# Kernel tuning notes

Measured on AMD Instinct MI355X. Metric: run time of the kernel, lower is better.

Reference implementation:

```python
import jax, jax.numpy as jnp
import numpy as np

CH_W = (1.0, 0.5, 2.0)  # channel_weights from init
NUM_NODES, FEAT_DIM, EMBED_DIM, B = 1_000_000, 128, 128, 200_000


def setup_inputs() -> dict:
    key = jax.random.key(0)
    ks = jax.random.split(key, 10)
    return {
        "nodes": jax.random.randint(ks[0], (B,), 0, NUM_NODES, dtype=jnp.int64 if jax.config.jax_enable_x64 else jnp.int32),
        "features": jax.random.normal(ks[1], (NUM_NODES, FEAT_DIM), dtype=jnp.float32),
        "neigh0": jax.random.normal(ks[2], (B, FEAT_DIM), dtype=jnp.float32),
        "neigh1": jax.random.normal(ks[3], (B, FEAT_DIM), dtype=jnp.float32),
        "neigh2": jax.random.normal(ks[4], (B, FEAT_DIM), dtype=jnp.float32),
        "W1": jax.random.normal(ks[5], (FEAT_DIM, 4 * FEAT_DIM), dtype=jnp.float32) * 0.05,
        "b1": jax.random.normal(ks[6], (FEAT_DIM,), dtype=jnp.float32) * 0.05,
        "W2": jax.random.normal(ks[7], (EMBED_DIM, FEAT_DIM), dtype=jnp.float32) * 0.05,
        "b2": jax.random.normal(ks[8], (EMBED_DIM,), dtype=jnp.float32) * 0.05,
    }


def reference(nodes, features, neigh0, neigh1, neigh2, W1, b1, W2, b2):
    # gather self embeddings: features(LongTensor(nodes))
    self_feats = features[nodes]                                   # [B, F]
    # per-channel weight scaling then concat: [B, (C+1)*F]
    combined = jnp.concatenate(
        [self_feats, neigh0 * CH_W[0], neigh1 * CH_W[1], neigh2 * CH_W[2]], axis=1
    )
    # Linear -> Tanh -> Linear (torch Linear: x @ W.T + b)
    h = jnp.tanh(combined @ W1.T + b1)                             # [B, F]
    return h @ W2.T + b2                                           # [B, E]
```

## Files before the change

kernel.cpp:

```cpp
#include <hip/hip_runtime.h>
#include <hip/hip_bf16.h>

typedef __attribute__((ext_vector_type(8))) short bf16x8;
typedef __attribute__((ext_vector_type(4))) float f32x4;

__device__ __forceinline__ unsigned short f2bf(float x){
  union { float f; unsigned int u; } a; a.f = x;
  unsigned int r = a.u + 0x7FFFu + ((a.u >> 16) & 1u);
  return (unsigned short)(r >> 16);
}

__device__ __forceinline__ void glds16(const void* g, void* l){
  __builtin_amdgcn_global_load_lds(
      (const __attribute__((address_space(1))) unsigned int*)g,
      (__attribute__((address_space(3))) unsigned int*)l,
      16, 0, 0);
}

__global__ void prep_w(const float* __restrict__ W1, const float* __restrict__ W2,
                       unsigned short* __restrict__ W1p, unsigned short* __restrict__ W2p){
  int t = blockIdx.x * 256 + threadIdx.x;
  int lane = t & 63;
  int lo = lane & 15, hi = lane >> 4;
  {
    int ktg = (t >> 6) & 15, nt = t >> 10;
    int c = ktg >> 2;
    int base = (c==0) ? 2 : ((c==1) ? 0 : 2*c);
    int P = base + ((ktg >> 1) & 1);
    int k2 = ktg & 1;
    float s = (c==2) ? 0.5f : ((c==3) ? 2.0f : 1.0f);
    int n = nt*16 + lo;
    int k = ktg*32 + hi*8;
    const float* src = W1 + n*512 + k;
    unsigned short* dst = W1p + ((size_t)((P*8 + nt)*2 + k2)*64 + lane)*8;
#pragma unroll
    for (int j=0;j<8;j++) dst[j] = f2bf(src[j]*s);
  }
  if (t < 2048){
    int kt = (t >> 6) & 3, nt = t >> 8;
    int n = nt*16 + lo;
    int k = kt*32 + hi*8;
    const float* src = W2 + n*128 + k;
    unsigned short* dst = W2p + (size_t)t*8;
#pragma unroll
    for (int j=0;j<8;j++) dst[j] = f2bf(src[j]);
  }
}

__device__ __forceinline__ void stage_neigh(char* db, int wv, int lane, int brow,
                                            const float* g, int half, int B){
  int r4 = lane >> 4, gs = lane & 15;
#pragma unroll
  for (int j=0;j<4;j++){
    int row = 4*(wv*4 + j) + r4;
    int gr = brow + row; gr = gr < B ? gr : (B-1);
    const char* src = (const char*)(g + (size_t)gr*128 + half*64) + ((gs ^ (row & 7)) << 4);
    glds16(src, db + row*256 + (gs << 4));
  }
}
__device__ __forceinline__ void stage_gather(char* db, int wv, int lane,
                                             const float* feat, const int* nid, int half){
  int r4 = lane >> 4, gs = lane & 15;
#pragma unroll
  for (int j=0;j<4;j++){
    int row = 4*(wv*4 + j) + r4;
    const char* src = (const char*)(feat + (size_t)nid[j]*128 + half*64) + ((gs ^ (row & 7)) << 4);
    glds16(src, db + row*256 + (gs << 4));
  }
}
__device__ __forceinline__ void stage_w(char* wb, int wv, int lane,
                                        const unsigned short* W1p, int P){
  const char* src = (const char*)W1p + (size_t)P*16384 + (wv*4)*1024 + (lane << 4);
#pragma unroll
  for (int j=0;j<4;j++)
    glds16(src + j*1024, wb + (wv*4 + j)*1024 + (lane << 4));
}

__device__ __forceinline__ void gemm_phase(const char* db, const char* wb,
    int wv, int lo, int hi, int lane, f32x4 acc[8])
{
  int row = wv*16 + lo;
  int s = row & 7;
  const char* rb = db + row*256;
  bf16x8 a[2];
#pragma unroll
  for (int k2=0;k2<2;k2++){
    int g0 = (8*k2 + 2*hi) ^ s;
    float4 x = *(const float4*)(rb + (g0 << 4));
    float4 y = *(const float4*)(rb + ((g0 ^ 1) << 4));
    bf16x8 t;
    t[0]=(short)f2bf(x.x); t[1]=(short)f2bf(x.y); t[2]=(short)f2bf(x.z); t[3]=(short)f2bf(x.w);
    t[4]=(short)f2bf(y.x); t[5]=(short)f2bf(y.y); t[6]=(short)f2bf(y.z); t[7]=(short)f2bf(y.w);
    a[k2] = t;
  }
#pragma unroll
  for (int nt=0;nt<8;nt++){
#pragma unroll
    for (int k2=0;k2<2;k2++){
      bf16x8 b = *(const bf16x8*)(wb + (((nt*2 + k2)*64 + lane) << 4));
      acc[nt] = __builtin_amdgcn_mfma_f32_16x16x32_bf16(a[k2], b, acc[nt], 0, 0, 0);
    }
  }
}

#define PH_WAIT8 asm volatile("s_waitcnt vmcnt(8)" ::: "memory")
#define PH_WAIT0 asm volatile("s_waitcnt vmcnt(0)" ::: "memory")
#define BAR do{ asm volatile("" ::: "memory"); __builtin_amdgcn_s_barrier(); \
                asm volatile("" ::: "memory"); }while(0)

__global__ __launch_bounds__(256, 2) void enc_main(
    const int* __restrict__ nodes, const float* __restrict__ feat,
    const float* __restrict__ g0, const float* __restrict__ g1,
    const float* __restrict__ g2,
    const unsigned short* __restrict__ W1p, const float* __restrict__ b1,
    const unsigned short* __restrict__ W2p, const float* __restrict__ b2,
    float* __restrict__ out, int B)
{
  __shared__ char smem[65536];
  char* DB0 = smem;            char* DB1 = smem + 16384;
  char* WB0 = smem + 32768;    char* WB1 = smem + 49152;

  const int tid  = threadIdx.x;
  const int lane = tid & 63;
  const int wv   = tid >> 6;
  const int lo   = lane & 15, hi = lane >> 4;
  const int brow = blockIdx.x * 64;

  float bb1[8];
#pragma unroll
  for (int nt=0;nt<8;nt++) bb1[nt] = b1[lo + 16*nt];
  int nid[4];
  {
    int r4 = lane >> 4;
#pragma unroll
    for (int j=0;j<4;j++){
      int r = brow + 4*(wv*4 + j) + r4;
      r = r < B ? r : (B-1);
      nid[j] = nodes[r];
    }
  }
  asm volatile("" ::: "memory");

  stage_neigh(DB0, wv, lane, brow, g0, 0, B);  stage_w(WB0, wv, lane, W1p, 0);
  stage_neigh(DB1, wv, lane, brow, g0, 1, B);  stage_w(WB1, wv, lane, W1p, 1);

  f32x4 acc[8];
#pragma unroll
  for (int nt=0;nt<8;nt++) acc[nt] = (f32x4){bb1[nt],bb1[nt],bb1[nt],bb1[nt]};

  PH_WAIT8; BAR;
  gemm_phase(DB0, WB0, wv, lo, hi, lane, acc);
  BAR;
  stage_gather(DB0, wv, lane, feat, nid, 0);   stage_w(WB0, wv, lane, W1p, 2);
  PH_WAIT8; BAR;
  gemm_phase(DB1, WB1, wv, lo, hi, lane, acc);
  BAR;
  stage_gather(DB1, wv, lane, feat, nid, 1);   stage_w(WB1, wv, lane, W1p, 3);
  PH_WAIT8; BAR;
  gemm_phase(DB0, WB0, wv, lo, hi, lane, acc);
  BAR;
  stage_neigh(DB0, wv, lane, brow, g1, 0, B);  stage_w(WB0, wv, lane, W1p, 4);
  PH_WAIT8; BAR;
  gemm_phase(DB1, WB1, wv, lo, hi, lane, acc);
  BAR;
  stage_neigh(DB1, wv, lane, brow, g1, 1, B);  stage_w(WB1, wv, lane, W1p, 5);
  PH_WAIT8; BAR;
  gemm_phase(DB0, WB0, wv, lo, hi, lane, acc);
  BAR;
  stage_neigh(DB0, wv, lane, brow, g2, 0, B);  stage_w(WB0, wv, lane, W1p, 6);
  PH_WAIT8; BAR;
  gemm_phase(DB1, WB1, wv, lo, hi, lane, acc);
  BAR;
  stage_neigh(DB1, wv, lane, brow, g2, 1, B);  stage_w(WB1, wv, lane, W1p, 7);
  PH_WAIT8; BAR;
  gemm_phase(DB0, WB0, wv, lo, hi, lane, acc);
  BAR;
  PH_WAIT0; BAR;
  gemm_phase(DB1, WB1, wv, lo, hi, lane, acc);

  char* hbase = WB0 + wv*4096;
#pragma unroll
  for (int nt=0;nt<8;nt++){
#pragma unroll
    for (int r=0;r<4;r++){
      float x = acc[nt][r];
      float t = 1.0f - 2.0f * __builtin_amdgcn_rcpf(__expf(2.0f*x) + 1.0f);
      int row = hi*4 + r;
      int colb = (lo + 16*nt)*2;
      *(unsigned short*)(hbase + row*256 + (colb ^ ((row & 7) << 4))) = f2bf(t);
    }
  }
  __syncthreads();

  const bf16x8* W2f = (const bf16x8*)W2p;
  f32x4 acc2[8];
#pragma unroll
  for (int nt=0;nt<8;nt++){ float v2 = b2[lo + 16*nt]; acc2[nt] = (f32x4){v2,v2,v2,v2}; }

  bf16x8 a2[4];
  {
    int row = lo;
    int swz = (row & 7) << 4;
#pragma unroll
    for (int kt=0;kt<4;kt++){
      int colb = kt*64 + hi*16;
      a2[kt] = *(const bf16x8*)(hbase + row*256 + (colb ^ swz));
    }
  }
#pragma unroll
  for (int nt=0;nt<8;nt++){
#pragma unroll
    for (int kt=0;kt<4;kt++){
      bf16x8 b = W2f[(nt*4 + kt)*64 + lane];
      acc2[nt] = __builtin_amdgcn_mfma_f32_16x16x32_bf16(a2[kt], b, acc2[nt], 0, 0, 0);
    }
  }

  int rbase = brow + wv*16 + hi*4;
#pragma unroll
  for (int r=0;r<4;r++){
    int gr = rbase + r;
    if (gr < B){
      float* op = out + (size_t)gr*128 + lo;
#pragma unroll
      for (int nt=0;nt<8;nt++) op[16*nt] = acc2[nt][r];
    }
  }
}

extern "C" void kernel_launch(void* const* d_in, const int* in_sizes, int n_in,
                              void* d_out, int out_size, void* d_ws, size_t ws_size,
                              hipStream_t stream) {
  const int*   nodes = (const int*)  d_in[0];
  const float* feat  = (const float*)d_in[1];
  const float* g0    = (const float*)d_in[2];
  const float* g1    = (const float*)d_in[3];
  const float* g2    = (const float*)d_in[4];
  const float* W1    = (const float*)d_in[5];
  const float* b1    = (const float*)d_in[6];
  const float* W2    = (const float*)d_in[7];
  const float* b2    = (const float*)d_in[8];
  float* out = (float*)d_out;
  const int B = in_sizes[0];

  unsigned short* W1p = (unsigned short*)d_ws;
  unsigned short* W2p = W1p + 8192*8;

  prep_w<<<32, 256, 0, stream>>>(W1, W2, W1p, W2p);
  int grid = (B + 63) / 64;
  enc_main<<<grid, 256, 0, stream>>>(nodes, feat, g0, g1, g2, W1p, b1, W2p, b2, out, B);
}
```

Measured before the change: 133.2 us.

## Split waves across output columns, keep W1 tiles in registers, triple-buffer activations

```diff
diff --git a/kernel.cpp b/kernel.cpp
--- a/kernel.cpp
+++ b/kernel.cpp
@@ -8,6 +8,11 @@
   union { float f; unsigned int u; } a; a.f = x;
   unsigned int r = a.u + 0x7FFFu + ((a.u >> 16) & 1u);
   return (unsigned short)(r >> 16);
+}
+__device__ __forceinline__ short bfc(float x){
+  __hip_bfloat16 h = __float2bfloat16(x);
+  union { __hip_bfloat16 h; short s; } u; u.h = h;
+  return u.s;
 }
 
 __device__ __forceinline__ void glds16(const void* g, void* l){
@@ -15,6 +20,9 @@
       (const __attribute__((address_space(1))) unsigned int*)g,
       (__attribute__((address_space(3))) unsigned int*)l,
       16, 0, 0);
+}
+__device__ __forceinline__ void gl16(bf16x8* d, const char* p){
+  asm volatile("global_load_dwordx4 %0, %1, off" : "=v"(*d) : "v"(p) : "memory");
 }
 
 __global__ void prep_w(const float* __restrict__ W1, const float* __restrict__ W2,
@@ -23,22 +31,23 @@
   int lane = t & 63;
   int lo = lane & 15, hi = lane >> 4;
   {
-    int ktg = (t >> 6) & 15, nt = t >> 10;
-    int c = ktg >> 2;
-    int base = (c==0) ? 2 : ((c==1) ? 0 : 2*c);
-    int P = base + ((ktg >> 1) & 1);
-    int k2 = ktg & 1;
-    float s = (c==2) ? 0.5f : ((c==3) ? 2.0f : 1.0f);
-    int n = nt*16 + lo;
+    int entry = t >> 6;
+    int k2 = entry & 1, nt2 = (entry>>1)&1, wv = (entry>>2)&3, P = entry>>4;
+    int pb = P >> 1;
+    int c = (pb==0) ? 1 : (pb==1) ? 0 : pb;
+    int ktg = c*4 + (P&1)*2 + k2;
+    float s = (c==2) ? 0.5f : (c==3) ? 2.0f : 1.0f;
+    int n = wv*32 + nt2*16 + lo;
     int k = ktg*32 + hi*8;
     const float* src = W1 + n*512 + k;
-    unsigned short* dst = W1p + ((size_t)((P*8 + nt)*2 + k2)*64 + lane)*8;
+    unsigned short* dst = W1p + (size_t)t*8;
 #pragma unroll
     for (int j=0;j<8;j++) dst[j] = f2bf(src[j]*s);
   }
   if (t < 2048){
-    int kt = (t >> 6) & 3, nt = t >> 8;
-    int n = nt*16 + lo;
+    int entry = t >> 6;
+    int kt = entry & 3, nt2 = (entry>>2)&1, wv = (entry>>3)&3;
+    int n = wv*32 + nt2*16 + lo;
     int k = kt*32 + hi*8;
     const float* src = W2 + n*128 + k;
     unsigned short* dst = W2p + (size_t)t*8;
@@ -68,47 +77,47 @@
     glds16(src, db + row*256 + (gs << 4));
   }
 }
-__device__ __forceinline__ void stage_w(char* wb, int wv, int lane,
-                                        const unsigned short* W1p, int P){
-  const char* src = (const char*)W1p + (size_t)P*16384 + (wv*4)*1024 + (lane << 4);
-#pragma unroll
-  for (int j=0;j<4;j++)
-    glds16(src + j*1024, wb + (wv*4 + j)*1024 + (lane << 4));
-}
-
-__device__ __forceinline__ void gemm_phase(const char* db, const char* wb,
-    int wv, int lo, int hi, int lane, f32x4 acc[8])
+__device__ __forceinline__ void loadW(bf16x8 w[2][2], const char* W1p, int wv, int lane, int P){
+  const char* base = W1p + (size_t)(P*4 + wv)*4096 + (lane << 4);
+  gl16(&w[0][0], base);
+  gl16(&w[0][1], base + 1024);
+  gl16(&w[1][0], base + 2048);
+  gl16(&w[1][1], base + 3072);
+}
+
+__device__ __forceinline__ void gemm_phase(const char* db, const bf16x8 w[2][2],
+    int lo, int hi, f32x4 acc[4][2])
 {
-  int row = wv*16 + lo;
-  int s = row & 7;
-  const char* rb = db + row*256;
-  bf16x8 a[2];
-#pragma unroll
-  for (int k2=0;k2<2;k2++){
-    int g0 = (8*k2 + 2*hi) ^ s;
-    float4 x = *(const float4*)(rb + (g0 << 4));
-    float4 y = *(const float4*)(rb + ((g0 ^ 1) << 4));
-    bf16x8 t;
-    t[0]=(short)f2bf(x.x); t[1]=(short)f2bf(x.y); t[2]=(short)f2bf(x.z); t[3]=(short)f2bf(x.w);
-    t[4]=(short)f2bf(y.x); t[5]=(short)f2bf(y.y); t[6]=(short)f2bf(y.z); t[7]=(short)f2bf(y.w);
-    a[k2] = t;
-  }
-#pragma unroll
-  for (int nt=0;nt<8;nt++){
+#pragma unroll
+  for (int rt=0;rt<4;rt++){
+    int row = rt*16 + lo;
+    int s = row & 7;
+    const char* rb = db + row*256;
+    bf16x8 a[2];
 #pragma unroll
     for (int k2=0;k2<2;k2++){
-      bf16x8 b = *(const bf16x8*)(wb + (((nt*2 + k2)*64 + lane) << 4));
-      acc[nt] = __builtin_amdgcn_mfma_f32_16x16x32_bf16(a[k2], b, acc[nt], 0, 0, 0);
-    }
-  }
-}
-
-#define PH_WAIT8 asm volatile("s_waitcnt vmcnt(8)" ::: "memory")
-#define PH_WAIT0 asm volatile("s_waitcnt vmcnt(0)" ::: "memory")
-#define BAR do{ asm volatile("" ::: "memory"); __builtin_amdgcn_s_barrier(); \
-                asm volatile("" ::: "memory"); }while(0)
-
-__global__ __launch_bounds__(256, 2) void enc_main(
+      int g0 = (8*k2 + 2*hi) ^ s;
+      float4 x = *(const float4*)(rb + (g0 << 4));
+      float4 y = *(const float4*)(rb + ((g0 ^ 1) << 4));
+      bf16x8 t;
+      t[0]=bfc(x.x); t[1]=bfc(x.y); t[2]=bfc(x.z); t[3]=bfc(x.w);
+      t[4]=bfc(y.x); t[5]=bfc(y.y); t[6]=bfc(y.z); t[7]=bfc(y.w);
+      a[k2] = t;
+    }
+#pragma unroll
+    for (int nt2=0;nt2<2;nt2++)
+#pragma unroll
+      for (int k2=0;k2<2;k2++)
+        acc[rt][nt2] = __builtin_amdgcn_mfma_f32_16x16x32_bf16(a[k2], w[nt2][k2], acc[rt][nt2], 0, 0, 0);
+  }
+}
+
+#define WAITN(n) do{ asm volatile("s_waitcnt vmcnt(" #n ")" ::: "memory"); \
+                     __builtin_amdgcn_sched_barrier(0); }while(0)
+#define BAR do{ __builtin_amdgcn_sched_barrier(0); __builtin_amdgcn_s_barrier(); \
+                __builtin_amdgcn_sched_barrier(0); }while(0)
+
+__global__ __launch_bounds__(256, 3) void enc_main(
     const int* __restrict__ nodes, const float* __restrict__ feat,
     const float* __restrict__ g0, const float* __restrict__ g1,
     const float* __restrict__ g2,
@@ -116,19 +125,18 @@
     const unsigned short* __restrict__ W2p, const float* __restrict__ b2,
     float* __restrict__ out, int B)
 {
-  __shared__ char smem[65536];
-  char* DB0 = smem;            char* DB1 = smem + 16384;
-  char* WB0 = smem + 32768;    char* WB1 = smem + 49152;
+  __shared__ char smem[49152];
+  char* DB0 = smem;  char* DB1 = smem + 16384;  char* DB2 = smem + 32768;
 
   const int tid  = threadIdx.x;
   const int lane = tid & 63;
   const int wv   = tid >> 6;
   const int lo   = lane & 15, hi = lane >> 4;
   const int brow = blockIdx.x * 64;
-
-  float bb1[8];
-#pragma unroll
-  for (int nt=0;nt<8;nt++) bb1[nt] = b1[lo + 16*nt];
+  const char* W1c = (const char*)W1p;
+
+  float bb1[2];
+  bb1[0] = b1[wv*32 + lo];  bb1[1] = b1[wv*32 + 16 + lo];
   int nid[4];
   {
     int r4 = lane >> 4;
@@ -139,91 +147,115 @@
       nid[j] = nodes[r];
     }
   }
-  asm volatile("" ::: "memory");
-
-  stage_neigh(DB0, wv, lane, brow, g0, 0, B);  stage_w(WB0, wv, lane, W1p, 0);
-  stage_neigh(DB1, wv, lane, brow, g0, 1, B);  stage_w(WB1, wv, lane, W1p, 1);
-
-  f32x4 acc[8];
-#pragma unroll
-  for (int nt=0;nt<8;nt++) acc[nt] = (f32x4){bb1[nt],bb1[nt],bb1[nt],bb1[nt]};
-
-  PH_WAIT8; BAR;
-  gemm_phase(DB0, WB0, wv, lo, hi, lane, acc);
-  BAR;
-  stage_gather(DB0, wv, lane, feat, nid, 0);   stage_w(WB0, wv, lane, W1p, 2);
-  PH_WAIT8; BAR;
-  gemm_phase(DB1, WB1, wv, lo, hi, lane, acc);
-  BAR;
-  stage_gather(DB1, wv, lane, feat, nid, 1);   stage_w(WB1, wv, lane, W1p, 3);
-  PH_WAIT8; BAR;
-  gemm_phase(DB0, WB0, wv, lo, hi, lane, acc);
-  BAR;
-  stage_neigh(DB0, wv, lane, brow, g1, 0, B);  stage_w(WB0, wv, lane, W1p, 4);
-  PH_WAIT8; BAR;
-  gemm_phase(DB1, WB1, wv, lo, hi, lane, acc);
-  BAR;
-  stage_neigh(DB1, wv, lane, brow, g1, 1, B);  stage_w(WB1, wv, lane, W1p, 5);
-  PH_WAIT8; BAR;
-  gemm_phase(DB0, WB0, wv, lo, hi, lane, acc);
-  BAR;
-  stage_neigh(DB0, wv, lane, brow, g2, 0, B);  stage_w(WB0, wv, lane, W1p, 6);
-  PH_WAIT8; BAR;
-  gemm_phase(DB1, WB1, wv, lo, hi, lane, acc);
-  BAR;
-  stage_neigh(DB1, wv, lane, brow, g2, 1, B);  stage_w(WB1, wv, lane, W1p, 7);
-  PH_WAIT8; BAR;
-  gemm_phase(DB0, WB0, wv, lo, hi, lane, acc);
-  BAR;
-  PH_WAIT0; BAR;
-  gemm_phase(DB1, WB1, wv, lo, hi, lane, acc);
-
-  char* hbase = WB0 + wv*4096;
-#pragma unroll
-  for (int nt=0;nt<8;nt++){
-#pragma unroll
-    for (int r=0;r<4;r++){
-      float x = acc[nt][r];
-      float t = 1.0f - 2.0f * __builtin_amdgcn_rcpf(__expf(2.0f*x) + 1.0f);
-      int row = hi*4 + r;
-      int colb = (lo + 16*nt)*2;
-      *(unsigned short*)(hbase + row*256 + (colb ^ ((row & 7) << 4))) = f2bf(t);
+  asm volatile("" :: "v"(nid[0]), "v"(nid[1]), "v"(nid[2]), "v"(nid[3]),
+                     "v"(bb1[0]), "v"(bb1[1]) : "memory");
+
+  bf16x8 w0[2][2], w1[2][2], w2[2][2];
+  stage_neigh(DB0, wv, lane, brow, g0, 0, B);
+  stage_neigh(DB1, wv, lane, brow, g0, 1, B);
+  loadW(w0, W1c, wv, lane, 0);
+  loadW(w1, W1c, wv, lane, 1);
+
+  f32x4 acc[4][2];
+#pragma unroll
+  for (int rt=0;rt<4;rt++)
+#pragma unroll
+    for (int nt2=0;nt2<2;nt2++)
+      acc[rt][nt2] = (f32x4){bb1[nt2],bb1[nt2],bb1[nt2],bb1[nt2]};
+
+  stage_gather(DB2, wv, lane, feat, nid, 0);
+  loadW(w2, W1c, wv, lane, 2);
+  WAITN(12); BAR;
+  gemm_phase(DB0, w0, lo, hi, acc);
+  BAR;
+  stage_gather(DB0, wv, lane, feat, nid, 1);
+  loadW(w0, W1c, wv, lane, 3);
+  WAITN(16); BAR;
+  gemm_phase(DB1, w1, lo, hi, acc);
+  BAR;
+  stage_neigh(DB1, wv, lane, brow, g1, 0, B);
+  loadW(w1, W1c, wv, lane, 4);
+  WAITN(16); BAR;
+  gemm_phase(DB2, w2, lo, hi, acc);
+  BAR;
+  stage_neigh(DB2, wv, lane, brow, g1, 1, B);
+  loadW(w2, W1c, wv, lane, 5);
+  WAITN(16); BAR;
+  gemm_phase(DB0, w0, lo, hi, acc);
+  BAR;
+  stage_neigh(DB0, wv, lane, brow, g2, 0, B);
+  loadW(w0, W1c, wv, lane, 6);
+  WAITN(16); BAR;
+  gemm_phase(DB1, w1, lo, hi, acc);
+  BAR;
+  stage_neigh(DB1, wv, lane, brow, g2, 1, B);
+  loadW(w1, W1c, wv, lane, 7);
+  WAITN(16); BAR;
+  gemm_phase(DB2, w2, lo, hi, acc);
+  BAR;
+  WAITN(8); BAR;
+  gemm_phase(DB0, w0, lo, hi, acc);
+  BAR;
+  WAITN(0); BAR;
+  gemm_phase(DB1, w1, lo, hi, acc);
+
+  const bf16x8* W2f = (const bf16x8*)W2p;
+  bf16x8 w2r[2][4];
+#pragma unroll
+  for (int nt2=0;nt2<2;nt2++)
+#pragma unroll
+    for (int kt=0;kt<4;kt++)
+      w2r[nt2][kt] = W2f[(size_t)((wv*2 + nt2)*4 + kt)*64 + lane];
+
+  char* hbase = smem;
+#pragma unroll
+  for (int rt=0;rt<4;rt++){
+#pragma unroll
+    for (int nt2=0;nt2<2;nt2++){
+#pragma unroll
+      for (int r=0;r<4;r++){
+        float x = acc[rt][nt2][r];
+        float t = 1.0f - 2.0f * __builtin_amdgcn_rcpf(__expf(2.0f*x) + 1.0f);
+        int row = rt*16 + hi*4 + r;
+        int colb = (wv*32 + nt2*16 + lo) * 2;
+        *(unsigned short*)(hbase + row*256 + (colb ^ ((row & 7) << 4))) = f2bf(t);
+      }
     }
   }
   __syncthreads();
 
-  const bf16x8* W2f = (const bf16x8*)W2p;
-  f32x4 acc2[8];
-#pragma unroll
-  for (int nt=0;nt<8;nt++){ float v2 = b2[lo + 16*nt]; acc2[nt] = (f32x4){v2,v2,v2,v2}; }
-
-  bf16x8 a2[4];
-  {
-    int row = lo;
+  float bb2[2];
+  bb2[0] = b2[wv*32 + lo];  bb2[1] = b2[wv*32 + 16 + lo];
+
+#pragma unroll
+  for (int rt=0;rt<4;rt++){
+    f32x4 acc2[2];
+    acc2[0] = (f32x4){bb2[0],bb2[0],bb2[0],bb2[0]};
+    acc2[1] = (f32x4){bb2[1],bb2[1],bb2[1],bb2[1]};
+    int row = rt*16 + lo;
     int swz = (row & 7) << 4;
+    const char* rb = hbase + row*256;
+    bf16x8 a2[4];
 #pragma unroll
     for (int kt=0;kt<4;kt++){
       int colb = kt*64 + hi*16;
-      a2[kt] = *(const bf16x8*)(hbase + row*256 + (colb ^ swz));
-    }
-  }
-#pragma unroll
-  for (int nt=0;nt<8;nt++){
-#pragma unroll
-    for (int kt=0;kt<4;kt++){
-      bf16x8 b = W2f[(nt*4 + kt)*64 + lane];
-      acc2[nt] = __builtin_amdgcn_mfma_f32_16x16x32_bf16(a2[kt], b, acc2[nt], 0, 0, 0);
-    }
-  }
-
-  int rbase = brow + wv*16 + hi*4;
-#pragma unroll
-  for (int r=0;r<4;r++){
-    int gr = rbase + r;
-    if (gr < B){
-      float* op = out + (size_t)gr*128 + lo;
-#pragma unroll
-      for (int nt=0;nt<8;nt++) op[16*nt] = acc2[nt][r];
+      a2[kt] = *(const bf16x8*)(rb + (colb ^ swz));
+    }
+#pragma unroll
+    for (int nt2=0;nt2<2;nt2++)
+#pragma unroll
+      for (int kt=0;kt<4;kt++)
+        acc2[nt2] = __builtin_amdgcn_mfma_f32_16x16x32_bf16(a2[kt], w2r[nt2][kt], acc2[nt2], 0, 0, 0);
+
+    int rbase = brow + rt*16 + hi*4;
+#pragma unroll
+    for (int r=0;r<4;r++){
+      int gr = rbase + r;
+      if (gr < B){
+        float* op = out + (size_t)gr*128 + wv*32 + lo;
+        op[0]  = acc2[0][r];
+        op[16] = acc2[1][r];
+      }
     }
   }
 }
```

Result: faster. 117.6 us (-11.7%).
